# Kernel optimization log

Measured on AMD Instinct MI355X. Metric: run time of the kernel, lower is better.

## Reference

```python
import jax, jax.numpy as jnp
import numpy as np

HIDDEN = 2048
KEY_DIM = 2048
NUM_HEADS = 16
EPS = 1e-05


def rms_norm(x, w, eps=EPS):
    ms = jnp.mean(x * x, axis=-1, keepdims=True)
    return x * jax.lax.rsqrt(ms + eps) * w


def setup_inputs() -> dict:
    key = jax.random.key(0)
    ks = jax.random.split(key, 6)
    bound = 1.0 / np.sqrt(HIDDEN)  # kaiming-uniform-ish scale
    x = jax.random.normal(ks[0], (2, 2048, HIDDEN), dtype=jnp.float32)
    rms_w = jnp.ones((HIDDEN,), dtype=jnp.float32)
    Wq = jax.random.uniform(ks[1], (HIDDEN, KEY_DIM), jnp.float32, -bound, bound)
    Wk = jax.random.uniform(ks[2], (HIDDEN, KEY_DIM), jnp.float32, -bound, bound)
    Wv = jax.random.uniform(ks[3], (HIDDEN, KEY_DIM), jnp.float32, -bound, bound)
    Wo = jax.random.uniform(ks[4], (KEY_DIM, HIDDEN), jnp.float32, -bound, bound)
    return {"x": x, "rms_w": rms_w, "Wq": Wq, "Wk": Wk, "Wv": Wv, "Wo": Wo}


def reference(x, rms_w, Wq, Wk, Wv, Wo):
    B, S, _ = x.shape
    residual = x
    xn = rms_norm(x, rms_w)
    # project and split heads: [B,S,H,Dh]
    q = (xn @ Wq).reshape(B, S, NUM_HEADS, KEY_DIM // NUM_HEADS)
    k = (xn @ Wk).reshape(B, S, NUM_HEADS, KEY_DIM // NUM_HEADS)
    v = (xn @ Wv).reshape(B, S, NUM_HEADS, KEY_DIM // NUM_HEADS)
    # NOTE: original scales by 1/sqrt(key_dim), not head_dim — kept faithful
    scale = 1.0 / jnp.sqrt(jnp.float32(KEY_DIM))
    scores = jnp.einsum('bshd,bthd->bhst', q, k) * scale  # [B,H,S,S]
    causal = jnp.tril(jnp.ones((S, S), dtype=bool))
    scores = jnp.where(causal[None, None], scores, -jnp.inf)
    probs = jax.nn.softmax(scores, axis=-1)  # stable max-subtract internally
    out = jnp.einsum('bhst,bthd->bshd', probs, v).reshape(B, S, KEY_DIM)
    return out @ Wo + residual
```

## Files before the change

### kernel.cpp

```cpp
#include <hip/hip_runtime.h>
#include <math.h>

typedef __attribute__((ext_vector_type(8))) short bf16x8;
typedef __attribute__((ext_vector_type(4))) float f32x4;
typedef __attribute__((ext_vector_type(16))) float f32x16;

#define HID 2048
#define SEQ 2048
#define NH  16
#define DH  128
#define QK_SCALE 0.02209708691207961f

__device__ __forceinline__ ushort f2bf(float f) {
  union { float f; unsigned u; } v; v.f = f;
  unsigned r = v.u + 0x7fffu + ((v.u >> 16) & 1u);
  return (ushort)(r >> 16);
}

__device__ __forceinline__ void gload16(const ushort* g, ushort* l) {
  __builtin_amdgcn_global_load_lds((const __attribute__((address_space(1))) void*)g,
                                   (__attribute__((address_space(3))) void*)l,
                                   16, 0, 0);
}

__global__ __launch_bounds__(256) void k_transpose(const float* __restrict__ W,
                                                   ushort* __restrict__ Wt) {
  __shared__ float t[32][33];
  int n0 = blockIdx.x * 32, k0 = blockIdx.y * 32;
  int tx = threadIdx.x, ty = threadIdx.y;
  for (int i = ty; i < 32; i += 8)
    t[i][tx] = W[(size_t)(k0 + i) * HID + n0 + tx];
  __syncthreads();
  for (int i = ty; i < 32; i += 8)
    Wt[(size_t)(n0 + i) * HID + k0 + tx] = f2bf(t[tx][i]);
}

__global__ __launch_bounds__(256) void k_rmsnorm(const float* __restrict__ x,
                                                 const float* __restrict__ w,
                                                 ushort* __restrict__ xn) {
  int row = blockIdx.x;
  const float* xr = x + (size_t)row * HID;
  int base = threadIdx.x * 8;
  float4 a = *(const float4*)(xr + base);
  float4 c = *(const float4*)(xr + base + 4);
  float ss = a.x*a.x + a.y*a.y + a.z*a.z + a.w*a.w
           + c.x*c.x + c.y*c.y + c.z*c.z + c.w*c.w;
  #pragma unroll
  for (int off = 32; off > 0; off >>= 1) ss += __shfl_xor(ss, off);
  __shared__ float red[4];
  if ((threadIdx.x & 63) == 0) red[threadIdx.x >> 6] = ss;
  __syncthreads();
  float tot = red[0] + red[1] + red[2] + red[3];
  float sc = rsqrtf(tot * (1.0f / HID) + 1e-5f);
  float4 wa = *(const float4*)(w + base);
  float4 wc = *(const float4*)(w + base + 4);
  ushort h[8];
  h[0] = f2bf(a.x * sc * wa.x); h[1] = f2bf(a.y * sc * wa.y);
  h[2] = f2bf(a.z * sc * wa.z); h[3] = f2bf(a.w * sc * wa.w);
  h[4] = f2bf(c.x * sc * wc.x); h[5] = f2bf(c.y * sc * wc.y);
  h[6] = f2bf(c.z * sc * wc.z); h[7] = f2bf(c.w * sc * wc.w);
  int4 pk;
  pk.x = h[0] | ((int)h[1] << 16);
  pk.y = h[2] | ((int)h[3] << 16);
  pk.z = h[4] | ((int)h[5] << 16);
  pk.w = h[6] | ((int)h[7] << 16);
  *(int4*)&xn[(size_t)row * HID + base] = pk;
}

template <int MODE>
__global__ __launch_bounds__(512, 2) void k_gemm2(const ushort* __restrict__ A,
                                                  const ushort* __restrict__ Bt,
                                                  ushort* __restrict__ obf,
                                                  ushort* __restrict__ vt,
                                                  float* __restrict__ ofl,
                                                  const float* __restrict__ resid) {
  constexpr int K = 2048, NS = 64;
  constexpr int NBN = (MODE == 0) ? 48 : 16;
  constexpr int QX = ((MODE == 0) ? 768 : 256) / 8;
  __shared__ ushort lds[4][12288];
  const int tid = threadIdx.x;
  const int lane = tid & 63, w = tid >> 6;
  const int wm = w >> 1, wn = w & 1;
  const int g = lane >> 4, l15 = lane & 15;
  const int swz = (blockIdx.x & 7) * QX + (blockIdx.x >> 3);
  const int bm = swz / NBN, bn = swz % NBN;

  f32x4 acc[4][4];
  #pragma unroll
  for (int i = 0; i < 4; ++i)
    #pragma unroll
    for (int j = 0; j < 4; ++j) acc[i][j] = f32x4{0.f, 0.f, 0.f, 0.f};

  auto STAGE = [&](int s) {
    const int ch = s & 3, k0 = s * 32;
    #pragma unroll
    for (int c = 0; c < 2; ++c) {
      int idx = c * 512 + tid;
      int r = idx >> 2, cp = idx & 3;
      int ck = cp ^ ((r >> 1) & 3);
      gload16(&A[(size_t)(bm * 256 + r) * K + k0 + ck * 8],
              &lds[ch][(c * 8 + w) * 512]);
    }
    {
      int r = tid >> 2, cp = tid & 3;
      int ck = cp ^ ((r >> 1) & 3);
      gload16(&Bt[(size_t)(bn * 128 + r) * K + k0 + ck * 8],
              &lds[ch][8192 + w * 512]);
    }
  };

  auto COMPUTE = [&](int s) {
    const ushort* La = lds[s & 3];
    const ushort* Lb = La + 8192;
    bf16x8 aF[4], bF[4];
    #pragma unroll
    for (int i = 0; i < 4; ++i) {
      int row = wm * 64 + i * 16 + l15;
      int cp = g ^ ((row >> 1) & 3);
      aF[i] = *(const bf16x8*)&La[row * 32 + cp * 8];
    }
    #pragma unroll
    for (int j = 0; j < 4; ++j) {
      int row = wn * 64 + j * 16 + l15;
      int cp = g ^ ((row >> 1) & 3);
      bF[j] = *(const bf16x8*)&Lb[row * 32 + cp * 8];
    }
    __builtin_amdgcn_s_setprio(1);
    #pragma unroll
    for (int i = 0; i < 4; ++i)
      #pragma unroll
      for (int j = 0; j < 4; ++j)
        acc[i][j] = __builtin_amdgcn_mfma_f32_16x16x32_bf16(aF[i], bF[j], acc[i][j], 0, 0, 0);
    __builtin_amdgcn_s_setprio(0);
  };

  STAGE(0); STAGE(1); STAGE(2);
  #pragma unroll 1
  for (int s = 0; s <= NS - 4; ++s) {
    asm volatile("s_waitcnt vmcnt(6)" ::: "memory");
    __builtin_amdgcn_s_barrier();
    __builtin_amdgcn_sched_barrier(0);
    STAGE(s + 3);
    COMPUTE(s);
  }
  asm volatile("s_waitcnt vmcnt(6)" ::: "memory");
  __builtin_amdgcn_s_barrier();
  __builtin_amdgcn_sched_barrier(0);
  COMPUTE(NS - 3);
  asm volatile("s_waitcnt vmcnt(3)" ::: "memory");
  __builtin_amdgcn_s_barrier();
  __builtin_amdgcn_sched_barrier(0);
  COMPUTE(NS - 2);
  asm volatile("s_waitcnt vmcnt(0)" ::: "memory");
  __builtin_amdgcn_s_barrier();
  __builtin_amdgcn_sched_barrier(0);
  COMPUTE(NS - 1);

  int rbase = bm * 256 + wm * 64 + g * 4;
  int cbase = bn * 128 + wn * 64 + l15;
  #pragma unroll
  for (int i = 0; i < 4; ++i) {
    #pragma unroll
    for (int j = 0; j < 4; ++j) {
      int col = cbase + j * 16;
      #pragma unroll
      for (int r = 0; r < 4; ++r) {
        int row = rbase + i * 16 + r;
        float v = acc[i][j][r];
        if (MODE == 0) {
          ushort hv = f2bf(v);
          if (col < 4096) {
            obf[(size_t)row * 4096 + col] = hv;
          } else {
            int nv = col - 4096;
            int h = nv >> 7, d = nv & 127;
            int b = row >> 11, s = row & 2047;
            vt[(size_t)((b * NH + h) * DH + d) * SEQ + s] = hv;
          }
        } else {
          ofl[(size_t)row * HID + col] = v + resid[(size_t)row * HID + col];
        }
      }
    }
  }
}

__global__ __launch_bounds__(256, 2) void k_attn2(const ushort* __restrict__ qk,
                                                  const ushort* __restrict__ vt,
                                                  ushort* __restrict__ aout) {
  __shared__ ushort sK[64 * 128];
  __shared__ ushort sV[128 * 64];
  const int tid = threadIdx.x;
  const int lane = tid & 63, w = tid >> 6;
  const int h2 = lane >> 5;
  const int l31 = lane & 31;
  const int bid = blockIdx.x;
  const int t = bid >> 3;
  const int bh = (bid & 7) + 8 * (t >> 4);
  const int qblk = 15 - (t & 15);
  const int b = bh >> 4, hh = bh & 15;
  const int q0w = qblk * 128 + w * 32;

  bf16x8 qf[8];
  {
    const ushort* qbase = qk + (size_t)(b * SEQ + q0w + l31) * 4096 + hh * DH;
    #pragma unroll
    for (int kk = 0; kk < 8; ++kk) qf[kk] = *(const bf16x8*)&qbase[kk * 16 + h2 * 8];
  }

  f32x16 accO[4];
  #pragma unroll
  for (int i = 0; i < 4; ++i)
    #pragma unroll
    for (int r = 0; r < 16; ++r) accO[i][r] = 0.f;
  float m_r = -1e30f, l_r = 0.f;

  const int ntile = 2 * qblk + 2;
  for (int tt = 0; tt < ntile; ++tt) {
    const int t0 = tt * 64;
    #pragma unroll
    for (int c = 0; c < 4; ++c) {
      int id = (w * 4 + c) * 64 + lane;
      int kr = id >> 4, ck = id & 15;
      gload16(qk + (size_t)(b * SEQ + t0 + kr) * 4096 + 2048 + hh * DH + ((ck ^ (kr & 7)) * 8),
              ((ushort*)sK) + (size_t)(w * 4 + c) * 512);
      int dr = id >> 3, cv = id & 7;
      gload16(vt + (size_t)(bh * DH + dr) * SEQ + t0 + ((cv ^ (dr & 7)) * 8),
              ((ushort*)sV) + (size_t)(w * 4 + c) * 512);
    }
    __syncthreads();

    if (t0 <= q0w + 31) {
      f32x16 accS[2];
      #pragma unroll
      for (int i = 0; i < 2; ++i)
        #pragma unroll
        for (int r = 0; r < 16; ++r) accS[i][r] = 0.f;
      #pragma unroll
      for (int kt = 0; kt < 2; ++kt) {
        const int row = kt * 32 + l31;
        #pragma unroll
        for (int kk = 0; kk < 8; ++kk) {
          const int cp = (kk * 2 + h2) ^ (lane & 7);
          bf16x8 kf = *(const bf16x8*)&sK[row * 128 + cp * 8];
          accS[kt] = __builtin_amdgcn_mfma_f32_32x32x16_bf16(kf, qf[kk], accS[kt], 0, 0, 0);
        }
      }
      const int qa = q0w + l31;
      float pmax = -INFINITY;
      if (t0 + 63 <= q0w) {
        #pragma unroll
        for (int kt = 0; kt < 2; ++kt)
          #pragma unroll
          for (int r = 0; r < 16; ++r) {
            float s = accS[kt][r] * QK_SCALE;
            accS[kt][r] = s;
            pmax = fmaxf(pmax, s);
          }
      } else {
        #pragma unroll
        for (int kt = 0; kt < 2; ++kt)
          #pragma unroll
          for (int r = 0; r < 16; ++r) {
            int ka = t0 + kt * 32 + (r & 3) + 8 * (r >> 2) + 4 * h2;
            float s = (ka <= qa) ? accS[kt][r] * QK_SCALE : -INFINITY;
            accS[kt][r] = s;
            pmax = fmaxf(pmax, s);
          }
      }
      pmax = fmaxf(pmax, __shfl_xor(pmax, 32));
      if (__any(pmax > m_r + 8.f)) {
        float mn = fmaxf(m_r, pmax);
        float al = __expf(m_r - mn);
        m_r = mn;
        l_r *= al;
        #pragma unroll
        for (int r = 0; r < 16; ++r) {
          float ar = __shfl(al, (r & 3) + 8 * (r >> 2) + 4 * h2);
          #pragma unroll
          for (int ds = 0; ds < 4; ++ds) accO[ds][r] *= ar;
        }
      }
      float rs = 0.f;
      #pragma unroll
      for (int kt = 0; kt < 2; ++kt)
        #pragma unroll
        for (int r = 0; r < 16; ++r) {
          float p = __expf(accS[kt][r] - m_r);
          rs += p;
          accS[kt][r] = p;
        }
      rs += __shfl_xor(rs, 32);
      l_r += rs;
      uint W[2][4][2];
      #pragma unroll
      for (int kt = 0; kt < 2; ++kt)
        #pragma unroll
        for (int bq = 0; bq < 4; ++bq)
          #pragma unroll
          for (int w2 = 0; w2 < 2; ++w2) {
            uint u0 = __float_as_uint(accS[kt][bq * 4 + w2 * 2]);
            uint u1 = __float_as_uint(accS[kt][bq * 4 + w2 * 2 + 1]);
            W[kt][bq][w2] = (u0 >> 16) | (u1 & 0xffff0000u);
          }
      #pragma unroll
      for (int kc = 0; kc < 4; ++kc) {
        const int kt = kc >> 1, pq = kc & 1;
        uint X0 = W[kt][2 * pq][0],     X1 = W[kt][2 * pq][1];
        uint Y0 = W[kt][2 * pq + 1][0], Y1 = W[kt][2 * pq + 1][1];
        uint sx0 = (uint)__shfl_xor((int)X0, 32);
        uint sx1 = (uint)__shfl_xor((int)X1, 32);
        uint sy0 = (uint)__shfl_xor((int)Y0, 32);
        uint sy1 = (uint)__shfl_xor((int)Y1, 32);
        union { uint u[4]; bf16x8 v; } pu;
        pu.u[0] = h2 ? sy0 : X0;
        pu.u[1] = h2 ? sy1 : X1;
        pu.u[2] = h2 ? Y0 : sx0;
        pu.u[3] = h2 ? Y1 : sx1;
        #pragma unroll
        for (int ds = 0; ds < 4; ++ds) {
          const int dr = ds * 32 + l31;
          const int cp = (kc * 2 + h2) ^ (lane & 7);
          bf16x8 vf = *(const bf16x8*)&sV[dr * 64 + cp * 8];
          accO[ds] = __builtin_amdgcn_mfma_f32_32x32x16_bf16(pu.v, vf, accO[ds], 0, 0, 0);
        }
      }
    }
    __syncthreads();
  }

  float linv = 1.f / l_r;
  #pragma unroll
  for (int r = 0; r < 16; ++r) {
    int qrel = (r & 3) + 8 * (r >> 2) + 4 * h2;
    float li = __shfl(linv, qrel);
    #pragma unroll
    for (int ds = 0; ds < 4; ++ds) {
      aout[(size_t)(b * SEQ + q0w + qrel) * HID + hh * DH + ds * 32 + l31] =
          f2bf(accO[ds][r] * li);
    }
  }
}

extern "C" void kernel_launch(void* const* d_in, const int* in_sizes, int n_in,
                              void* d_out, int out_size, void* d_ws, size_t ws_size,
                              hipStream_t stream) {
  const float* x     = (const float*)d_in[0];
  const float* rms_w = (const float*)d_in[1];
  const float* Wq    = (const float*)d_in[2];
  const float* Wk    = (const float*)d_in[3];
  const float* Wv    = (const float*)d_in[4];
  const float* Wo    = (const float*)d_in[5];
  float* out = (float*)d_out;

  char* ws = (char*)d_ws;
  ushort* WqkvT = (ushort*)ws; ws += (size_t)6144 * 2048 * 2;
  ushort* WoT   = (ushort*)ws; ws += (size_t)2048 * 2048 * 2;
  ushort* xn    = (ushort*)ws; ws += (size_t)4096 * 2048 * 2;
  ushort* qkbuf = (ushort*)ws; ws += (size_t)4096 * 4096 * 2;
  ushort* vt    = (ushort*)ws; ws += (size_t)4096 * 2048 * 2;
  ushort* aout  = (ushort*)ws; ws += (size_t)4096 * 2048 * 2;

  dim3 tb(32, 8), tg(64, 64);
  k_transpose<<<tg, tb, 0, stream>>>(Wq, WqkvT);
  k_transpose<<<tg, tb, 0, stream>>>(Wk, WqkvT + (size_t)2048 * 2048);
  k_transpose<<<tg, tb, 0, stream>>>(Wv, WqkvT + (size_t)4096 * 2048);
  k_transpose<<<tg, tb, 0, stream>>>(Wo, WoT);

  k_rmsnorm<<<4096, 256, 0, stream>>>(x, rms_w, xn);

  k_gemm2<0><<<768, 512, 0, stream>>>(xn, WqkvT, qkbuf, vt, nullptr, nullptr);

  k_attn2<<<512, 256, 0, stream>>>(qkbuf, vt, aout);

  k_gemm2<1><<<256, 512, 0, stream>>>(aout, WoT, nullptr, nullptr, out, x);
}
```

Baseline: 293.3 us.

## Restructure GEMM main loop into interleaved half-tile MFMA and load ping-pong schedule

Rewrites the GEMM K-loop from a 4-slot, 32-wide stage pipeline into a double buffer of 64-wide tiles, each split into two 32-wide halves. LDS reads, async global-to-LDS loads and half-sized MFMA groups are interleaved with extra barriers and explicit lgkmcnt waits, and the LDS swizzle changes from (row>>1)&3 to row&3. The aim is better overlap of memory traffic with MFMA issue. The cost is twice as many barriers per K step and a more fragile hand-written schedule.

```diff
diff --git a/kernel.cpp b/kernel.cpp
--- a/kernel.cpp
+++ b/kernel.cpp
@@ -22,6 +22,11 @@
                                    (__attribute__((address_space(3))) void*)l,
                                    16, 0, 0);
 }
+
+#define VMCNT(n) asm volatile("s_waitcnt vmcnt(" #n ")" ::: "memory")
+#define LGKM0()  do { asm volatile("s_waitcnt lgkmcnt(0)" ::: "memory"); \
+                      __builtin_amdgcn_sched_barrier(0); } while (0)
+#define BAR()    __builtin_amdgcn_s_barrier()
 
 __global__ __launch_bounds__(256) void k_transpose(const float* __restrict__ W,
                                                    ushort* __restrict__ Wt) {
@@ -68,16 +73,16 @@
 }
 
 template <int MODE>
-__global__ __launch_bounds__(512, 2) void k_gemm2(const ushort* __restrict__ A,
+__global__ __launch_bounds__(512, 2) void k_gemm3(const ushort* __restrict__ A,
                                                   const ushort* __restrict__ Bt,
                                                   ushort* __restrict__ obf,
                                                   ushort* __restrict__ vt,
                                                   float* __restrict__ ofl,
                                                   const float* __restrict__ resid) {
-  constexpr int K = 2048, NS = 64;
+  constexpr int K = 2048;
   constexpr int NBN = (MODE == 0) ? 48 : 16;
   constexpr int QX = ((MODE == 0) ? 768 : 256) / 8;
-  __shared__ ushort lds[4][12288];
+  __shared__ ushort lds[49152];
   const int tid = threadIdx.x;
   const int lane = tid & 63, w = tid >> 6;
   const int wm = w >> 1, wn = w & 1;
@@ -90,71 +95,75 @@
   for (int i = 0; i < 4; ++i)
     #pragma unroll
     for (int j = 0; j < 4; ++j) acc[i][j] = f32x4{0.f, 0.f, 0.f, 0.f};
-
-  auto STAGE = [&](int s) {
-    const int ch = s & 3, k0 = s * 32;
-    #pragma unroll
-    for (int c = 0; c < 2; ++c) {
-      int idx = c * 512 + tid;
-      int r = idx >> 2, cp = idx & 3;
-      int ck = cp ^ ((r >> 1) & 3);
-      gload16(&A[(size_t)(bm * 256 + r) * K + k0 + ck * 8],
-              &lds[ch][(c * 8 + w) * 512]);
-    }
-    {
-      int r = tid >> 2, cp = tid & 3;
-      int ck = cp ^ ((r >> 1) & 3);
-      gload16(&Bt[(size_t)(bn * 128 + r) * K + k0 + ck * 8],
-              &lds[ch][8192 + w * 512]);
-    }
-  };
-
-  auto COMPUTE = [&](int s) {
-    const ushort* La = lds[s & 3];
-    const ushort* Lb = La + 8192;
-    bf16x8 aF[4], bF[4];
+  bf16x8 aF[4], bF[4];
+
+  auto dsA = [&](int buf, int kk) {
+    const ushort* base = lds + (buf * 2 + kk) * 8192;
     #pragma unroll
     for (int i = 0; i < 4; ++i) {
       int row = wm * 64 + i * 16 + l15;
-      int cp = g ^ ((row >> 1) & 3);
-      aF[i] = *(const bf16x8*)&La[row * 32 + cp * 8];
-    }
+      aF[i] = *(const bf16x8*)&base[row * 32 + ((g ^ (row & 3)) * 8)];
+    }
+  };
+  auto dsB = [&](int buf, int kk) {
+    const ushort* base = lds + 32768 + (buf * 2 + kk) * 4096;
     #pragma unroll
     for (int j = 0; j < 4; ++j) {
       int row = wn * 64 + j * 16 + l15;
-      int cp = g ^ ((row >> 1) & 3);
-      bF[j] = *(const bf16x8*)&Lb[row * 32 + cp * 8];
-    }
+      bF[j] = *(const bf16x8*)&base[row * 32 + ((g ^ (row & 3)) * 8)];
+    }
+  };
+  auto stA = [&](int buf, int kk, int t2) {
+    ushort* base = lds + (buf * 2 + kk) * 8192;
+    #pragma unroll
+    for (int L = 0; L < 2; ++L) {
+      int r = (L * 8 + w) * 16 + (lane >> 2);
+      int ck = (lane & 3) ^ (r & 3);
+      gload16(&A[(size_t)(bm * 256 + r) * K + t2 * 64 + kk * 32 + ck * 8],
+              base + (L * 8 + w) * 512);
+    }
+  };
+  auto stB = [&](int buf, int kk, int t2) {
+    ushort* base = lds + 32768 + (buf * 2 + kk) * 4096;
+    int r = w * 16 + (lane >> 2);
+    int ck = (lane & 3) ^ (r & 3);
+    gload16(&Bt[(size_t)(bn * 128 + r) * K + t2 * 64 + kk * 32 + ck * 8],
+            base + w * 512);
+  };
+  auto MF = [&](int ih) {
     __builtin_amdgcn_s_setprio(1);
     #pragma unroll
-    for (int i = 0; i < 4; ++i)
+    for (int i = 0; i < 2; ++i)
       #pragma unroll
       for (int j = 0; j < 4; ++j)
-        acc[i][j] = __builtin_amdgcn_mfma_f32_16x16x32_bf16(aF[i], bF[j], acc[i][j], 0, 0, 0);
+        acc[ih * 2 + i][j] =
+            __builtin_amdgcn_mfma_f32_16x16x32_bf16(aF[ih * 2 + i], bF[j],
+                                                    acc[ih * 2 + i][j], 0, 0, 0);
     __builtin_amdgcn_s_setprio(0);
   };
 
-  STAGE(0); STAGE(1); STAGE(2);
+  stA(0, 0, 0); stB(0, 0, 0); stA(0, 1, 0); stB(0, 1, 0); stA(1, 0, 1); stB(1, 0, 1);
+  VMCNT(6); BAR();
+
   #pragma unroll 1
-  for (int s = 0; s <= NS - 4; ++s) {
-    asm volatile("s_waitcnt vmcnt(6)" ::: "memory");
-    __builtin_amdgcn_s_barrier();
-    __builtin_amdgcn_sched_barrier(0);
-    STAGE(s + 3);
-    COMPUTE(s);
-  }
-  asm volatile("s_waitcnt vmcnt(6)" ::: "memory");
-  __builtin_amdgcn_s_barrier();
-  __builtin_amdgcn_sched_barrier(0);
-  COMPUTE(NS - 3);
-  asm volatile("s_waitcnt vmcnt(3)" ::: "memory");
-  __builtin_amdgcn_s_barrier();
-  __builtin_amdgcn_sched_barrier(0);
-  COMPUTE(NS - 2);
-  asm volatile("s_waitcnt vmcnt(0)" ::: "memory");
-  __builtin_amdgcn_s_barrier();
-  __builtin_amdgcn_sched_barrier(0);
-  COMPUTE(NS - 1);
+  for (int t = 0; t < 30; t += 2) {
+    dsA(0, 0); dsB(0, 0); stA(1, 1, t + 1); LGKM0(); MF(0); BAR();
+    stB(1, 1, t + 1); MF(1); VMCNT(6); BAR();
+    dsA(0, 1); dsB(0, 1); stA(0, 0, t + 2); LGKM0(); MF(0); BAR();
+    stB(0, 0, t + 2); MF(1); VMCNT(6); BAR();
+    dsA(1, 0); dsB(1, 0); stA(0, 1, t + 2); LGKM0(); MF(0); BAR();
+    stB(0, 1, t + 2); MF(1); VMCNT(6); BAR();
+    dsA(1, 1); dsB(1, 1); stA(1, 0, t + 3); LGKM0(); MF(0); BAR();
+    stB(1, 0, t + 3); MF(1); VMCNT(6); BAR();
+  }
+  dsA(0, 0); dsB(0, 0); stA(1, 1, 31); LGKM0(); MF(0); BAR();
+  stB(1, 1, 31); MF(1); VMCNT(6); BAR();
+  dsA(0, 1); dsB(0, 1); LGKM0(); MF(0); BAR();
+  MF(1); VMCNT(3); BAR();
+  dsA(1, 0); dsB(1, 0); LGKM0(); MF(0); BAR();
+  MF(1); VMCNT(0); BAR();
+  dsA(1, 1); dsB(1, 1); LGKM0(); MF(0); BAR();
+  MF(1);
 
   int rbase = bm * 256 + wm * 64 + g * 4;
   int cbase = bn * 128 + wn * 64 + l15;
@@ -369,9 +378,9 @@
 
   k_rmsnorm<<<4096, 256, 0, stream>>>(x, rms_w, xn);
 
-  k_gemm2<0><<<768, 512, 0, stream>>>(xn, WqkvT, qkbuf, vt, nullptr, nullptr);
+  k_gemm3<0><<<768, 512, 0, stream>>>(xn, WqkvT, qkbuf, vt, nullptr, nullptr);
 
   k_attn2<<<512, 256, 0, stream>>>(qkbuf, vt, aout);
 
-  k_gemm2<1><<<256, 512, 0, stream>>>(aout, WoT, nullptr, nullptr, out, x);
-}
+  k_gemm3<1><<<256, 512, 0, stream>>>(aout, WoT, nullptr, nullptr, out, x);
+}
```

Result: no change. 298.3 us (+1.7%).
